# Kernel tuning notes

Hardware: AMD Instinct MI355X
Metric: run time of the kernel (lower is better)

The kernel has to match this reference:

```python
import jax, jax.numpy as jnp
import numpy as np

B, C, L = 4, 256, 4096
H = 8
DK = C // H


def setup_inputs() -> dict:
    key = jax.random.key(0)
    kx, kq, kk, kv, kl = jax.random.split(key, 5)
    scale = 1.0 / np.sqrt(C)
    return {
        "x": jax.random.normal(kx, (B, C, L), dtype=jnp.float32),
        "Wq": jax.random.normal(kq, (C, C), dtype=jnp.float32) * scale,
        "Wk": jax.random.normal(kk, (C, C), dtype=jnp.float32) * scale,
        "Wv": jax.random.normal(kv, (C, C), dtype=jnp.float32) * scale,
        "Wl": jax.random.normal(kl, (C, C), dtype=jnp.float32) * scale,
    }


def reference(x, Wq, Wk, Wv, Wl):
    # Conv1d with kernel_size=1, no bias == channel-mixing matmul per position.
    def proj(W, t):  # W: [C_out, C_in], t: [B, C_in, L] -> [B, L, H, DK]
        y = jnp.einsum('oc,bcl->blo', W, t)
        return y.reshape(B, L, H, DK)

    q = proj(Wq, x)  # [B, L, H, DK]
    k = proj(Wk, x)
    v = proj(Wv, x)

    # scores: [B, H, L, L]
    scores = jnp.einsum('bqhd,bkhd->bhqk', q, k) / jnp.sqrt(jnp.float32(DK))
    p_attn = jax.nn.softmax(scores, axis=-1)
    # attention output with post-ReLU: [B, L, H, DK] -> [B, L, C]
    out = jax.nn.relu(jnp.einsum('bhqk,bkhd->bqhd', p_attn, v)).reshape(B, L, C)
    # last_conv: [B, C_out, L]
    return jnp.einsum('oc,blc->bol', Wl, out)
```

## Files before the change

kernel.cpp:

```cpp
#include <hip/hip_runtime.h>

#define L_DIM 4096
#define C_DIM 256
#define B_DIM 4
#define NH 8
#define DK 32

#define QSCALE 0.25507694f

typedef __bf16 bf16x8 __attribute__((ext_vector_type(8)));
typedef float  f32x4  __attribute__((ext_vector_type(4)));
typedef float  f32x16 __attribute__((ext_vector_type(16)));

static __device__ __forceinline__ unsigned pk_bf16(float lo, float hi) {
    unsigned a = __builtin_bit_cast(unsigned, lo) + 0x8000u;
    unsigned b = __builtin_bit_cast(unsigned, hi) + 0x8000u;
    return __builtin_amdgcn_perm(b, a, 0x07060302u);
}

__global__ __launch_bounds__(256) void transpose_x_kernel(
    const float* __restrict__ x, __bf16* __restrict__ xt)
{
    const int t  = threadIdx.x;
    const int l0 = blockIdx.x * 64;
    const int c0 = blockIdx.y * 64;
    const int b  = blockIdx.z;

    __shared__ __attribute__((aligned(16))) float T[64][65];

    {
        const int r  = t >> 2;
        const int lc = (t & 3) * 16;
        const float* xp = x + ((size_t)b * C_DIM + c0 + r) * L_DIM + l0 + lc;
        #pragma unroll
        for (int k = 0; k < 4; ++k)
            *(f32x4*)&T[r][lc + k * 4] = *(const f32x4*)(xp + k * 4);
    }
    __syncthreads();
    {
        const int l  = t >> 2;
        const int cc = (t & 3) * 16;
        unsigned u[8];
        #pragma unroll
        for (int i = 0; i < 8; ++i)
            u[i] = pk_bf16(T[cc + 2 * i][l], T[cc + 2 * i + 1][l]);
        __bf16* op = xt + ((size_t)b * L_DIM + l0 + l) * C_DIM + c0 + cc;
        *(uint4*)op       = make_uint4(u[0], u[1], u[2], u[3]);
        *(uint4*)(op + 8) = make_uint4(u[4], u[5], u[6], u[7]);
    }
}

__global__ __launch_bounds__(256) void proj_mfma_kernel(
    const __bf16* __restrict__ xt, const float* __restrict__ Wq,
    const float* __restrict__ Wk, const float* __restrict__ Wv,
    __bf16* __restrict__ Qb, __bf16* __restrict__ Kb, __bf16* __restrict__ Vb)
{
    const int t    = threadIdx.x;
    const int wave = t >> 6;
    const int lane = t & 63;
    const int n32  = lane & 31;
    const int hl   = lane >> 5;
    const int l0   = blockIdx.x * 128;
    const int ob   = blockIdx.y & 1;
    const int p    = blockIdx.y >> 1;
    const int b    = blockIdx.z;
    const float* W = (p == 0) ? Wq : ((p == 1) ? Wk : Wv);
    const float sc = (p == 0) ? QSCALE : 1.0f;

    __shared__ __attribute__((aligned(16))) __bf16 Wt[128][72];
    __shared__ __attribute__((aligned(16))) __bf16 Xs[128][72];

    const int wo  = t >> 1, wcc = (t & 1) * 32;
    const int xl  = t >> 1, xcc = (t & 1) * 32;
    const float*  wg = W + (size_t)(ob * 128 + wo) * C_DIM + wcc;
    const __bf16* xg = xt + ((size_t)b * L_DIM + l0 + xl) * C_DIM + xcc;

    const int moff = (wave & 1) * 64;
    const int noff = (wave >> 1) * 64;

    f32x16 acc[2][2];
    #pragma unroll
    for (int i = 0; i < 2; ++i)
        #pragma unroll
        for (int j = 0; j < 2; ++j)
            #pragma unroll
            for (int r = 0; r < 16; ++r) acc[i][j][r] = 0.f;

    unsigned wpk[16];
    bf16x8   xpr[4];
    #pragma unroll
    for (int k = 0; k < 8; ++k) {
        f32x4 wv = *(const f32x4*)(wg + k * 4);
        wpk[k * 2]     = pk_bf16(wv[0] * sc, wv[1] * sc);
        wpk[k * 2 + 1] = pk_bf16(wv[2] * sc, wv[3] * sc);
    }
    #pragma unroll
    for (int g = 0; g < 4; ++g) xpr[g] = *(const bf16x8*)(xg + g * 8);

    for (int bk = 0; bk < 4; ++bk) {
        __syncthreads();
        #pragma unroll
        for (int g = 0; g < 4; ++g) {
            *(uint4*)&Wt[wo][wcc + g * 8] =
                make_uint4(wpk[g*4], wpk[g*4+1], wpk[g*4+2], wpk[g*4+3]);
            *(bf16x8*)&Xs[xl][xcc + g * 8] = xpr[g];
        }
        if (bk < 3) {
            #pragma unroll
            for (int k = 0; k < 8; ++k) {
                f32x4 wv = *(const f32x4*)(wg + (bk + 1) * 64 + k * 4);
                wpk[k * 2]     = pk_bf16(wv[0] * sc, wv[1] * sc);
                wpk[k * 2 + 1] = pk_bf16(wv[2] * sc, wv[3] * sc);
            }
            #pragma unroll
            for (int g = 0; g < 4; ++g)
                xpr[g] = *(const bf16x8*)(xg + (bk + 1) * 64 + g * 8);
        }
        __syncthreads();

        #pragma unroll
        for (int ks = 0; ks < 4; ++ks) {
            bf16x8 a0 = *(const bf16x8*)&Wt[moff + n32     ][ks * 16 + hl * 8];
            bf16x8 a1 = *(const bf16x8*)&Wt[moff + 32 + n32][ks * 16 + hl * 8];
            bf16x8 b0 = *(const bf16x8*)&Xs[noff + n32     ][ks * 16 + hl * 8];
            bf16x8 b1 = *(const bf16x8*)&Xs[noff + 32 + n32][ks * 16 + hl * 8];
            acc[0][0] = __builtin_amdgcn_mfma_f32_32x32x16_bf16(a0, b0, acc[0][0], 0, 0, 0);
            acc[0][1] = __builtin_amdgcn_mfma_f32_32x32x16_bf16(a0, b1, acc[0][1], 0, 0, 0);
            acc[1][0] = __builtin_amdgcn_mfma_f32_32x32x16_bf16(a1, b0, acc[1][0], 0, 0, 0);
            acc[1][1] = __builtin_amdgcn_mfma_f32_32x32x16_bf16(a1, b1, acc[1][1], 0, 0, 0);
        }
    }

    #pragma unroll
    for (int mt = 0; mt < 2; ++mt) {
        const int o32 = ob * 128 + moff + mt * 32;
        const int h   = o32 >> 5;
        const int bh  = b * NH + h;
        #pragma unroll
        for (int nt = 0; nt < 2; ++nt) {
            const int l = l0 + noff + nt * 32 + n32;
            if (p < 2) {
                __bf16* out = ((p == 0) ? Qb : Kb) + ((size_t)bh * L_DIM + l) * DK;
                #pragma unroll
                for (int g = 0; g < 4; ++g) {
                    unsigned u0 = pk_bf16(acc[mt][nt][g*4],     acc[mt][nt][g*4+1]);
                    unsigned u1 = pk_bf16(acc[mt][nt][g*4+2],   acc[mt][nt][g*4+3]);
                    *(uint2*)(out + 4 * hl + 8 * g) = make_uint2(u0, u1);
                }
            } else {
                #pragma unroll
                for (int r = 0; r < 16; ++r) {
                    const int dk = (r & 3) + 4 * hl + 8 * (r >> 2);
                    Vb[((size_t)bh * DK + dk) * L_DIM + l] = (__bf16)acc[mt][nt][r];
                }
            }
        }
    }
}

__global__ __launch_bounds__(256) void attn_kernel(
    const __bf16* __restrict__ Q, const __bf16* __restrict__ K,
    const __bf16* __restrict__ V, __bf16* __restrict__ At)
{
    const int tid  = threadIdx.x;
    const int wave = tid >> 6;
    const int lane = tid & 63;
    const int n32  = lane & 31;
    const int hl   = lane >> 5;
    const int h    = blockIdx.y;
    const int b    = blockIdx.z;
    const int bh   = b * NH + h;
    const int q0   = blockIdx.x * 256 + wave * 64;

    __shared__ __attribute__((aligned(16))) __bf16 Ks[64][40];
    __shared__ __attribute__((aligned(16))) __bf16 Vs[32][72];

    bf16x8 qf[2][2];
    #pragma unroll
    for (int qt = 0; qt < 2; ++qt) {
        const __bf16* qp = Q + ((size_t)bh * L_DIM + q0 + qt * 32 + n32) * DK;
        qf[qt][0] = *(const bf16x8*)(qp + hl * 8);
        qf[qt][1] = *(const bf16x8*)(qp + 16 + hl * 8);
    }

    f32x16 oacc[2], lacc[2];
    #pragma unroll
    for (int qt = 0; qt < 2; ++qt)
        #pragma unroll
        for (int r = 0; r < 16; ++r) { oacc[qt][r] = 0.f; lacc[qt][r] = 0.f; }

    const f32x16 z16 = {};

    bf16x8 ones;
    #pragma unroll
    for (int j = 0; j < 8; ++j) ones[j] = (__bf16)1.0f;

    const __bf16* kg = K + (size_t)bh * L_DIM * DK + (tid >> 2) * DK + (tid & 3) * 8;
    const __bf16* vg = V + ((size_t)bh * DK + (tid >> 3)) * L_DIM + (tid & 7) * 8;
    __bf16* ksd = &Ks[tid >> 2][(tid & 3) * 8];
    const int va  = tid & 7;
    __bf16* vsd0 = &Vs[tid >> 3][(va >> 1) * 16 + (va & 1) * 4];
    __bf16* vsd1 = vsd0 + 8;

    bf16x8 kreg = *(const bf16x8*)kg;
    bf16x8 vreg = *(const bf16x8*)vg;

    for (int kt = 0; kt < L_DIM / 64; ++kt) {
        __syncthreads();
        *(bf16x8*)ksd = kreg;
        union { bf16x8 v; uint2 u2[2]; } vv; vv.v = vreg;
        *(uint2*)vsd0 = vv.u2[0];
        *(uint2*)vsd1 = vv.u2[1];
        {
            const int nkt = (kt + 1) & (L_DIM / 64 - 1);
            kreg = *(const bf16x8*)(kg + (size_t)nkt * 64 * DK);
            vreg = *(const bf16x8*)(vg + nkt * 64);
        }
        __syncthreads();

        bf16x8 kf[2][2];
        kf[0][0] = *(const bf16x8*)&Ks[n32     ][hl * 8];
        kf[0][1] = *(const bf16x8*)&Ks[n32     ][16 + hl * 8];
        kf[1][0] = *(const bf16x8*)&Ks[32 + n32][hl * 8];
        kf[1][1] = *(const bf16x8*)&Ks[32 + n32][16 + hl * 8];
        bf16x8 vf[4];
        vf[0] = *(const bf16x8*)&Vs[n32][     hl * 8];
        vf[1] = *(const bf16x8*)&Vs[n32][16 + hl * 8];
        vf[2] = *(const bf16x8*)&Vs[n32][32 + hl * 8];
        vf[3] = *(const bf16x8*)&Vs[n32][48 + hl * 8];

        #pragma unroll
        for (int mt = 0; mt < 2; ++mt) {
            #pragma unroll
            for (int qt = 0; qt < 2; ++qt) {
                f32x16 s = __builtin_amdgcn_mfma_f32_32x32x16_bf16(
                    kf[mt][0], qf[qt][0], z16, 0, 0, 0);
                s = __builtin_amdgcn_mfma_f32_32x32x16_bf16(
                    kf[mt][1], qf[qt][1], s, 0, 0, 0);

                float e[16];
                #pragma unroll
                for (int r = 0; r < 16; ++r) e[r] = __builtin_amdgcn_exp2f(s[r]);
                union { unsigned u[4]; bf16x8 v; } p0, p1;
                #pragma unroll
                for (int i = 0; i < 4; ++i) {
                    p0.u[i] = pk_bf16(e[2 * i],     e[2 * i + 1]);
                    p1.u[i] = pk_bf16(e[8 + 2 * i], e[8 + 2 * i + 1]);
                }

                oacc[qt] = __builtin_amdgcn_mfma_f32_32x32x16_bf16(
                    vf[mt * 2],     p0.v, oacc[qt], 0, 0, 0);
                lacc[qt] = __builtin_amdgcn_mfma_f32_32x32x16_bf16(
                    ones,           p0.v, lacc[qt], 0, 0, 0);
                oacc[qt] = __builtin_amdgcn_mfma_f32_32x32x16_bf16(
                    vf[mt * 2 + 1], p1.v, oacc[qt], 0, 0, 0);
                lacc[qt] = __builtin_amdgcn_mfma_f32_32x32x16_bf16(
                    ones,           p1.v, lacc[qt], 0, 0, 0);
            }
        }
    }

    #pragma unroll
    for (int qt = 0; qt < 2; ++qt) {
        const float inv = __builtin_amdgcn_rcpf(lacc[qt][0]);
        __bf16* ap = At + ((size_t)b * L_DIM + q0 + qt * 32 + n32) * C_DIM
                        + h * 32 + 4 * hl;
        #pragma unroll
        for (int g = 0; g < 4; ++g) {
            float v0 = oacc[qt][g*4]   * inv; v0 = v0 > 0.f ? v0 : 0.f;
            float v1 = oacc[qt][g*4+1] * inv; v1 = v1 > 0.f ? v1 : 0.f;
            float v2 = oacc[qt][g*4+2] * inv; v2 = v2 > 0.f ? v2 : 0.f;
            float v3 = oacc[qt][g*4+3] * inv; v3 = v3 > 0.f ? v3 : 0.f;
            *(uint2*)(ap + 8 * g) = make_uint2(pk_bf16(v0, v1), pk_bf16(v2, v3));
        }
    }
}

__global__ __launch_bounds__(256) void final_mfma_kernel(
    const __bf16* __restrict__ at, const float* __restrict__ Wl,
    float* __restrict__ y)
{
    const int t    = threadIdx.x;
    const int wave = t >> 6;
    const int lane = t & 63;
    const int n32  = lane & 31;
    const int hl   = lane >> 5;
    const int l0   = blockIdx.x * 64;
    const int ob   = blockIdx.y;
    const int b    = blockIdx.z;

    __shared__ __attribute__((aligned(16))) __bf16 Wt[128][72];
    __shared__ __attribute__((aligned(16))) __bf16 Xs[64][72];

    const int wo  = t >> 1, wcc = (t & 1) * 32;
    const int xl  = t >> 2, xcc = (t & 3) * 16;
    const float*  wg = Wl + (size_t)(ob * 128 + wo) * C_DIM + wcc;
    const __bf16* xg = at + ((size_t)b * L_DIM + l0 + xl) * C_DIM + xcc;

    const int moff = (wave & 1) * 64;
    const int noff = (wave >> 1) * 32;

    f32x16 acc[2];
    #pragma unroll
    for (int i = 0; i < 2; ++i)
        #pragma unroll
        for (int r = 0; r < 16; ++r) acc[i][r] = 0.f;

    unsigned wpk[16];
    bf16x8   xpr[2];
    #pragma unroll
    for (int k = 0; k < 8; ++k) {
        f32x4 wv = *(const f32x4*)(wg + k * 4);
        wpk[k * 2]     = pk_bf16(wv[0], wv[1]);
        wpk[k * 2 + 1] = pk_bf16(wv[2], wv[3]);
    }
    #pragma unroll
    for (int g = 0; g < 2; ++g) xpr[g] = *(const bf16x8*)(xg + g * 8);

    for (int bk = 0; bk < 4; ++bk) {
        __syncthreads();
        #pragma unroll
        for (int g = 0; g < 4; ++g)
            *(uint4*)&Wt[wo][wcc + g * 8] =
                make_uint4(wpk[g*4], wpk[g*4+1], wpk[g*4+2], wpk[g*4+3]);
        #pragma unroll
        for (int g = 0; g < 2; ++g)
            *(bf16x8*)&Xs[xl][xcc + g * 8] = xpr[g];
        if (bk < 3) {
            #pragma unroll
            for (int k = 0; k < 8; ++k) {
                f32x4 wv = *(const f32x4*)(wg + (bk + 1) * 64 + k * 4);
                wpk[k * 2]     = pk_bf16(wv[0], wv[1]);
                wpk[k * 2 + 1] = pk_bf16(wv[2], wv[3]);
            }
            #pragma unroll
            for (int g = 0; g < 2; ++g)
                xpr[g] = *(const bf16x8*)(xg + (bk + 1) * 64 + g * 8);
        }
        __syncthreads();

        #pragma unroll
        for (int ks = 0; ks < 4; ++ks) {
            bf16x8 a0 = *(const bf16x8*)&Wt[moff + n32     ][ks * 16 + hl * 8];
            bf16x8 a1 = *(const bf16x8*)&Wt[moff + 32 + n32][ks * 16 + hl * 8];
            bf16x8 b0 = *(const bf16x8*)&Xs[noff + n32     ][ks * 16 + hl * 8];
            acc[0] = __builtin_amdgcn_mfma_f32_32x32x16_bf16(a0, b0, acc[0], 0, 0, 0);
            acc[1] = __builtin_amdgcn_mfma_f32_32x32x16_bf16(a1, b0, acc[1], 0, 0, 0);
        }
    }

    #pragma unroll
    for (int mt = 0; mt < 2; ++mt) {
        #pragma unroll
        for (int r = 0; r < 16; ++r) {
            const int o = ob * 128 + moff + mt * 32 + (r & 3) + 4 * hl + 8 * (r >> 2);
            y[((size_t)b * C_DIM + o) * L_DIM + l0 + noff + n32] = acc[mt][r];
        }
    }
}

extern "C" void kernel_launch(void* const* d_in, const int* in_sizes, int n_in,
                              void* d_out, int out_size, void* d_ws, size_t ws_size,
                              hipStream_t stream)
{
    const float* x  = (const float*)d_in[0];
    const float* Wq = (const float*)d_in[1];
    const float* Wk = (const float*)d_in[2];
    const float* Wv = (const float*)d_in[3];
    const float* Wl = (const float*)d_in[4];
    float* y = (float*)d_out;

    const size_t n = (size_t)B_DIM * NH * L_DIM * DK;
    __bf16* Xt = (__bf16*)d_ws;
    __bf16* Qb = Xt + n;
    __bf16* Kb = Qb + n;
    __bf16* Vb = Kb + n;
    __bf16* At = Vb + n;

    transpose_x_kernel<<<dim3(L_DIM/64, C_DIM/64, B_DIM), 256, 0, stream>>>(x, Xt);
    proj_mfma_kernel<<<dim3(L_DIM/128, 6, B_DIM), 256, 0, stream>>>(
        Xt, Wq, Wk, Wv, Qb, Kb, Vb);
    attn_kernel<<<dim3(L_DIM/256, NH, B_DIM), 256, 0, stream>>>(Qb, Kb, Vb, At);
    final_mfma_kernel<<<dim3(L_DIM/64, 2, B_DIM), 256, 0, stream>>>(At, Wl, y);
}
```

Measured before the change: 220.0 us.

## Split attention over two key halves and merge partials in final projection

Doubles the attention grid by splitting the key sequence into two halves per block. Each half writes an unnormalized bf16 partial output and its row sums. The final projection kernel sums the partials, normalizes, and applies ReLU while staging into shared memory. The aim is better CU occupancy and latency hiding in attention, at the cost of extra global traffic and bf16 rounding of the partial sums.

New measurement: 216.3 us. Within noise of the previous version (-1.7%).

```diff
diff --git a/kernel.cpp b/kernel.cpp
--- a/kernel.cpp
+++ b/kernel.cpp
@@ -160,17 +160,20 @@
 
 __global__ __launch_bounds__(256) void attn_kernel(
     const __bf16* __restrict__ Q, const __bf16* __restrict__ K,
-    const __bf16* __restrict__ V, __bf16* __restrict__ At)
+    const __bf16* __restrict__ V, __bf16* __restrict__ Op0,
+    __bf16* __restrict__ Op1, float* __restrict__ Ls)
 {
-    const int tid  = threadIdx.x;
-    const int wave = tid >> 6;
-    const int lane = tid & 63;
-    const int n32  = lane & 31;
-    const int hl   = lane >> 5;
-    const int h    = blockIdx.y;
-    const int b    = blockIdx.z;
-    const int bh   = b * NH + h;
-    const int q0   = blockIdx.x * 256 + wave * 64;
+    const int tid   = threadIdx.x;
+    const int wave  = tid >> 6;
+    const int lane  = tid & 63;
+    const int n32   = lane & 31;
+    const int hl    = lane >> 5;
+    const int h     = blockIdx.y;
+    const int b     = blockIdx.z >> 1;
+    const int khalf = blockIdx.z & 1;
+    const int bh    = b * NH + h;
+    const int q0    = blockIdx.x * 256 + wave * 64;
+    const int kt0   = khalf * 32;
 
     __shared__ __attribute__((aligned(16))) __bf16 Ks[64][40];
     __shared__ __attribute__((aligned(16))) __bf16 Vs[32][72];
@@ -202,17 +205,17 @@
     __bf16* vsd0 = &Vs[tid >> 3][(va >> 1) * 16 + (va & 1) * 4];
     __bf16* vsd1 = vsd0 + 8;
 
-    bf16x8 kreg = *(const bf16x8*)kg;
-    bf16x8 vreg = *(const bf16x8*)vg;
-
-    for (int kt = 0; kt < L_DIM / 64; ++kt) {
+    bf16x8 kreg = *(const bf16x8*)(kg + (size_t)kt0 * 64 * DK);
+    bf16x8 vreg = *(const bf16x8*)(vg + kt0 * 64);
+
+    for (int kt = 0; kt < 32; ++kt) {
         __syncthreads();
         *(bf16x8*)ksd = kreg;
         union { bf16x8 v; uint2 u2[2]; } vv; vv.v = vreg;
         *(uint2*)vsd0 = vv.u2[0];
         *(uint2*)vsd1 = vv.u2[1];
         {
-            const int nkt = (kt + 1) & (L_DIM / 64 - 1);
+            const int nkt = kt0 + ((kt + 1) & 31);
             kreg = *(const bf16x8*)(kg + (size_t)nkt * 64 * DK);
             vreg = *(const bf16x8*)(vg + nkt * 64);
         }
@@ -260,24 +263,24 @@
         }
     }
 
+    __bf16* Op = khalf ? Op1 : Op0;
     #pragma unroll
     for (int qt = 0; qt < 2; ++qt) {
-        const float inv = __builtin_amdgcn_rcpf(lacc[qt][0]);
-        __bf16* ap = At + ((size_t)b * L_DIM + q0 + qt * 32 + n32) * C_DIM
-                        + h * 32 + 4 * hl;
+        const int l = q0 + qt * 32 + n32;
+        __bf16* ap = Op + ((size_t)b * L_DIM + l) * C_DIM + h * 32 + 4 * hl;
         #pragma unroll
         for (int g = 0; g < 4; ++g) {
-            float v0 = oacc[qt][g*4]   * inv; v0 = v0 > 0.f ? v0 : 0.f;
-            float v1 = oacc[qt][g*4+1] * inv; v1 = v1 > 0.f ? v1 : 0.f;
-            float v2 = oacc[qt][g*4+2] * inv; v2 = v2 > 0.f ? v2 : 0.f;
-            float v3 = oacc[qt][g*4+3] * inv; v3 = v3 > 0.f ? v3 : 0.f;
-            *(uint2*)(ap + 8 * g) = make_uint2(pk_bf16(v0, v1), pk_bf16(v2, v3));
-        }
+            *(uint2*)(ap + 8 * g) = make_uint2(
+                pk_bf16(oacc[qt][g*4],     oacc[qt][g*4+1]),
+                pk_bf16(oacc[qt][g*4+2],   oacc[qt][g*4+3]));
+        }
+        Ls[((size_t)khalf * B_DIM * NH + bh) * L_DIM + l] = lacc[qt][0];
     }
 }
 
 __global__ __launch_bounds__(256) void final_mfma_kernel(
-    const __bf16* __restrict__ at, const float* __restrict__ Wl,
+    const __bf16* __restrict__ Op0, const __bf16* __restrict__ Op1,
+    const float* __restrict__ Ls, const float* __restrict__ Wl,
     float* __restrict__ y)
 {
     const int t    = threadIdx.x;
@@ -294,8 +297,20 @@
 
     const int wo  = t >> 1, wcc = (t & 1) * 32;
     const int xl  = t >> 2, xcc = (t & 3) * 16;
-    const float*  wg = Wl + (size_t)(ob * 128 + wo) * C_DIM + wcc;
-    const __bf16* xg = at + ((size_t)b * L_DIM + l0 + xl) * C_DIM + xcc;
+    const float* wg = Wl + (size_t)(ob * 128 + wo) * C_DIM + wcc;
+    const size_t obase = ((size_t)b * L_DIM + l0 + xl) * C_DIM + xcc;
+
+    float inv[4];
+    {
+        const int lidx = l0 + xl;
+        #pragma unroll
+        for (int bk = 0; bk < 4; ++bk) {
+            const int hh = (bk * 64 + xcc) >> 5;
+            const float l1 = Ls[((size_t)0 * B_DIM * NH + b * NH + hh) * L_DIM + lidx];
+            const float l2 = Ls[((size_t)1 * B_DIM * NH + b * NH + hh) * L_DIM + lidx];
+            inv[bk] = __builtin_amdgcn_rcpf(l1 + l2);
+        }
+    }
 
     const int moff = (wave & 1) * 64;
     const int noff = (wave >> 1) * 32;
@@ -307,15 +322,17 @@
         for (int r = 0; r < 16; ++r) acc[i][r] = 0.f;
 
     unsigned wpk[16];
-    bf16x8   xpr[2];
+    bf16x8   o1r, o2r;
     #pragma unroll
     for (int k = 0; k < 8; ++k) {
         f32x4 wv = *(const f32x4*)(wg + k * 4);
         wpk[k * 2]     = pk_bf16(wv[0], wv[1]);
         wpk[k * 2 + 1] = pk_bf16(wv[2], wv[3]);
     }
-    #pragma unroll
-    for (int g = 0; g < 2; ++g) xpr[g] = *(const bf16x8*)(xg + g * 8);
+    o1r = *(const bf16x8*)(Op0 + obase);
+    o2r = *(const bf16x8*)(Op1 + obase);
+    bf16x8 o1r2 = *(const bf16x8*)(Op0 + obase + 8);
+    bf16x8 o2r2 = *(const bf16x8*)(Op1 + obase + 8);
 
     for (int bk = 0; bk < 4; ++bk) {
         __syncthreads();
@@ -323,9 +340,27 @@
         for (int g = 0; g < 4; ++g)
             *(uint4*)&Wt[wo][wcc + g * 8] =
                 make_uint4(wpk[g*4], wpk[g*4+1], wpk[g*4+2], wpk[g*4+3]);
-        #pragma unroll
-        for (int g = 0; g < 2; ++g)
-            *(bf16x8*)&Xs[xl][xcc + g * 8] = xpr[g];
+        {
+            unsigned u[4];
+            #pragma unroll
+            for (int i = 0; i < 4; ++i) {
+                float v0 = ((float)o1r[2*i]   + (float)o2r[2*i]  ) * inv[bk];
+                float v1 = ((float)o1r[2*i+1] + (float)o2r[2*i+1]) * inv[bk];
+                v0 = v0 > 0.f ? v0 : 0.f;
+                v1 = v1 > 0.f ? v1 : 0.f;
+                u[i] = pk_bf16(v0, v1);
+            }
+            *(uint4*)&Xs[xl][xcc] = make_uint4(u[0], u[1], u[2], u[3]);
+            #pragma unroll
+            for (int i = 0; i < 4; ++i) {
+                float v0 = ((float)o1r2[2*i]   + (float)o2r2[2*i]  ) * inv[bk];
+                float v1 = ((float)o1r2[2*i+1] + (float)o2r2[2*i+1]) * inv[bk];
+                v0 = v0 > 0.f ? v0 : 0.f;
+                v1 = v1 > 0.f ? v1 : 0.f;
+                u[i] = pk_bf16(v0, v1);
+            }
+            *(uint4*)&Xs[xl][xcc + 8] = make_uint4(u[0], u[1], u[2], u[3]);
+        }
         if (bk < 3) {
             #pragma unroll
             for (int k = 0; k < 8; ++k) {
@@ -333,9 +368,10 @@
                 wpk[k * 2]     = pk_bf16(wv[0], wv[1]);
                 wpk[k * 2 + 1] = pk_bf16(wv[2], wv[3]);
             }
-            #pragma unroll
-            for (int g = 0; g < 2; ++g)
-                xpr[g] = *(const bf16x8*)(xg + (bk + 1) * 64 + g * 8);
+            o1r  = *(const bf16x8*)(Op0 + obase + (bk + 1) * 64);
+            o2r  = *(const bf16x8*)(Op1 + obase + (bk + 1) * 64);
+            o1r2 = *(const bf16x8*)(Op0 + obase + (bk + 1) * 64 + 8);
+            o2r2 = *(const bf16x8*)(Op1 + obase + (bk + 1) * 64 + 8);
         }
         __syncthreads();
 
@@ -371,15 +407,19 @@
     float* y = (float*)d_out;
 
     const size_t n = (size_t)B_DIM * NH * L_DIM * DK;
-    __bf16* Xt = (__bf16*)d_ws;
-    __bf16* Qb = Xt + n;
-    __bf16* Kb = Qb + n;
-    __bf16* Vb = Kb + n;
-    __bf16* At = Vb + n;
+    __bf16* Qb  = (__bf16*)d_ws;
+    __bf16* Kb  = Qb + n;
+    __bf16* Vb  = Kb + n;
+    __bf16* Xt  = Vb + n;
+    __bf16* Op0 = Xt;
+    __bf16* Op1 = Xt + n;
+    float*  Ls  = (float*)(Op1 + n);
 
     transpose_x_kernel<<<dim3(L_DIM/64, C_DIM/64, B_DIM), 256, 0, stream>>>(x, Xt);
     proj_mfma_kernel<<<dim3(L_DIM/128, 6, B_DIM), 256, 0, stream>>>(
         Xt, Wq, Wk, Wv, Qb, Kb, Vb);
-    attn_kernel<<<dim3(L_DIM/256, NH, B_DIM), 256, 0, stream>>>(Qb, Kb, Vb, At);
-    final_mfma_kernel<<<dim3(L_DIM/64, 2, B_DIM), 256, 0, stream>>>(At, Wl, y);
-}
+    attn_kernel<<<dim3(L_DIM/256, NH, B_DIM * 2), 256, 0, stream>>>(
+        Qb, Kb, Vb, Op0, Op1, Ls);
+    final_mfma_kernel<<<dim3(L_DIM/64, 2, B_DIM), 256, 0, stream>>>(
+        Op0, Op1, Ls, Wl, y);
+}
```
